# Kernel optimization log

Hardware: AMD Instinct MI355X
Metric: run time of the kernel (lower is better)

Reference implementation:

```python
import jax, jax.numpy as jnp
import numpy as np

_IDENTITY = jnp.array([1, 0, 0, 0], dtype=jnp.float32)

G, T, P, B = 512, 128, 256, 512  # num_graphs, max_terms, n_params, batch


def setup_inputs() -> dict:
    key = jax.random.key(0)
    k0, k1, k2, k3, k4 = jax.random.split(key, 5)
    psi_const = jax.random.randint(k0, (G, T), 0, 2).astype(jnp.int32)
    psi_params = jax.random.randint(k1, (G, T, P), 0, 2).astype(jnp.float32)
    phi_const = jax.random.randint(k2, (G, T), 0, 2).astype(jnp.int32)
    phi_params = jax.random.randint(k3, (G, T, P), 0, 2).astype(jnp.float32)
    param_vals = jax.random.randint(k4, (B, P), 0, 2).astype(jnp.float32)
    return {
        "psi_const": psi_const,
        "psi_params": psi_params,
        "phi_const": phi_const,
        "phi_params": phi_params,
        "param_vals": param_vals,
    }


def reference(psi_const, psi_params, phi_const, phi_params, param_vals):
    # GF(2) matmul: contract bitmasks with binary parameter values, mod 2.
    # psi_params: (G,T,P), param_vals: (B,P) -> (B,G,T)
    psi = jnp.mod(psi_const[None].astype(jnp.float32)
                  + jnp.einsum("gtp,bp->bgt", psi_params, param_vals), 2.0)
    phi = jnp.mod(phi_const[None].astype(jnp.float32)
                  + jnp.einsum("gtp,bp->bgt", phi_params, param_vals), 2.0)
    # Elementwise parity product and mod-2 sum over terms -> (B,G)
    exponent = jnp.mod(psi * phi, 2.0)
    sum_exponents = jnp.mod(jnp.sum(exponent, axis=-1), 2.0)
    # Parity-to-sign: (-1)^e = 1 - 2e, embedded as exact scalar (B,G,4)
    summands_exact = (1.0 - 2.0 * sum_exponents)[..., None] * _IDENTITY
    return summands_exact
```

## Files before the change

### kernel.cpp

```cpp
#include <hip/hip_runtime.h>

typedef unsigned long long u64;

#define G 512
#define T 128
#define P 256
#define B 512

struct __align__(16) U64x2 { u64 x, y; };

__global__ __launch_bounds__(256) void pack_pv_kernel(
    const float* __restrict__ pv, u64* __restrict__ out)
{
    int lane = threadIdx.x & 63;
    int wave = threadIdx.x >> 6;
    int row  = blockIdx.x * 4 + wave;
    const float4* src = (const float4*)(pv + (size_t)row * P);
    float4 f = src[lane];
    u64 w0 = __ballot(f.x != 0.0f);
    u64 w1 = __ballot(f.y != 0.0f);
    u64 w2 = __ballot(f.z != 0.0f);
    u64 w3 = __ballot(f.w != 0.0f);
    if (lane == 0) {
        U64x2* d = (U64x2*)(out + row * 4);
        U64x2 a; a.x = w0; a.y = w1;
        U64x2 c; c.x = w2; c.y = w3;
        d[0] = a;
        d[1] = c;
    }
}

__global__ __launch_bounds__(256) void pack_codes_kernel(
    const int* __restrict__ psi_c, const int* __restrict__ phi_c,
    u64* __restrict__ codes)
{
    int lane = threadIdx.x & 63;
    int wave = threadIdx.x >> 6;
    int g = blockIdx.x * 4 + wave;
    u64 a0 = __ballot(psi_c[g * T + lane]      != 0);
    u64 a1 = __ballot(psi_c[g * T + 64 + lane] != 0);
    u64 b0 = __ballot(phi_c[g * T + lane]      != 0);
    u64 b1 = __ballot(phi_c[g * T + 64 + lane] != 0);
    if (lane == 0) {
        U64x2* d = (U64x2*)(codes + g * 4);
        U64x2 x; x.x = a0; x.y = a1;
        U64x2 y; y.x = b0; y.y = b1;
        d[0] = x;
        d[1] = y;
    }
}

__global__ __launch_bounds__(256) void pack_mat_kernel(
    const float* __restrict__ psi, const float* __restrict__ phi,
    u64* __restrict__ rows)
{
    int lane = threadIdx.x & 63;
    int wave = threadIdx.x >> 6;
    int wid  = blockIdx.x * 4 + wave;
    #pragma unroll 4
    for (int j = 0; j < 16; ++j) {
        int item = wid * 16 + j;
        int m = item >> 16;
        int r = item & 65535;
        const float* mat = m ? phi : psi;
        const float4* src = (const float4*)(mat + (size_t)r * P);
        float4 f = src[lane];
        u64 w0 = __ballot(f.x != 0.0f);
        u64 w1 = __ballot(f.y != 0.0f);
        u64 w2 = __ballot(f.z != 0.0f);
        u64 w3 = __ballot(f.w != 0.0f);
        if (lane == 0) {
            U64x2* d = (U64x2*)(rows + (size_t)r * 8 + m * 4);
            U64x2 a; a.x = w0; a.y = w1;
            U64x2 c; c.x = w2; c.y = w3;
            d[0] = a;
            d[1] = c;
        }
    }
}

__global__ __launch_bounds__(256) void pi_main_kernel(
    const u64* __restrict__ rows,
    const u64* __restrict__ codes,
    const u64* __restrict__ pv,
    float4*    __restrict__ out)
{
    const int g = blockIdx.x >> 1;
    const int b = ((blockIdx.x & 1) << 8) | threadIdx.x;

    const u64* v = pv + (size_t)b * 4;
    u64 v0 = v[0], v1 = v[1], v2 = v[2], v3 = v[3];

    const u64* rp = rows + (size_t)g * (T * 8);

    unsigned e = 0;
    for (int blk = 0; blk < 2; ++blk) {
        u64 pcw = codes[g * 4 + blk];
        u64 qcw = codes[g * 4 + 2 + blk];
        const u64* r = rp + blk * 64 * 8;
        #pragma unroll 4
        for (int i = 0; i < 64; ++i, r += 8) {
            u64 ma = (r[0] & v0) ^ (r[1] & v1) ^ (r[2] & v2) ^ (r[3] & v3);
            u64 mb = (r[4] & v0) ^ (r[5] & v1) ^ (r[6] & v2) ^ (r[7] & v3);
            unsigned pa = (unsigned)__popcll(ma) ^ (unsigned)(pcw >> i);
            unsigned pb = (unsigned)__popcll(mb) ^ (unsigned)(qcw >> i);
            e ^= pa & pb;
        }
    }
    e &= 1u;

    float s = 1.0f - 2.0f * (float)e;
    out[(size_t)b * G + g] = make_float4(s, 0.0f, 0.0f, 0.0f);
}

extern "C" void kernel_launch(void* const* d_in, const int* in_sizes, int n_in,
                              void* d_out, int out_size, void* d_ws, size_t ws_size,
                              hipStream_t stream) {
    const int*   psi_const  = (const int*)  d_in[0];
    const float* psi_params = (const float*)d_in[1];
    const int*   phi_const  = (const int*)  d_in[2];
    const float* phi_params = (const float*)d_in[3];
    const float* param_vals = (const float*)d_in[4];

    u64* ws    = (u64*)d_ws;
    u64* rows  = ws;
    u64* codes = ws + (size_t)G * T * 8;
    u64* pv    = codes + (size_t)G * 4;

    pack_pv_kernel   <<<B / 4, 256, 0, stream>>>(param_vals, pv);
    pack_codes_kernel<<<G / 4, 256, 0, stream>>>(psi_const, phi_const, codes);
    pack_mat_kernel  <<<2048,  256, 0, stream>>>(psi_params, phi_params, rows);
    pi_main_kernel   <<<G * 2, 256, 0, stream>>>(rows, codes, pv, (float4*)d_out);
}
```

Baseline: 196.2 us.

## Pack bitmasks per-thread via exponent bit, merge small packers, split terms across halves

Packing no longer uses wave ballots. Each thread reads 32 contiguous floats and builds a 32-bit word from bit 29 of each float, which only works for exact 0.0/1.0 inputs. The two small packing kernels are merged into one launch, cutting a kernel launch. The main kernel now uses four blocks per graph and splits the 128 terms between two thread halves, whose partial parities are combined through shared memory. The goal is more parallelism and better packing bandwidth, at the cost of a sync and relying on the binary-valued inputs.

```diff
diff --git a/kernel.cpp b/kernel.cpp
--- a/kernel.cpp
+++ b/kernel.cpp
@@ -1,81 +1,77 @@
 #include <hip/hip_runtime.h>
 
 typedef unsigned long long u64;
+typedef unsigned int u32;
 
 #define G 512
 #define T 128
 #define P 256
 #define B 512
+#define NROWS 65536
 
-struct __align__(16) U64x2 { u64 x, y; };
 
-__global__ __launch_bounds__(256) void pack_pv_kernel(
-    const float* __restrict__ pv, u64* __restrict__ out)
+__global__ __launch_bounds__(256) void pack_big_kernel(
+    const float* __restrict__ psi, const float* __restrict__ phi,
+    u32* __restrict__ rows)
 {
-    int lane = threadIdx.x & 63;
-    int wave = threadIdx.x >> 6;
-    int row  = blockIdx.x * 4 + wave;
-    const float4* src = (const float4*)(pv + (size_t)row * P);
-    float4 f = src[lane];
-    u64 w0 = __ballot(f.x != 0.0f);
-    u64 w1 = __ballot(f.y != 0.0f);
-    u64 w2 = __ballot(f.z != 0.0f);
-    u64 w3 = __ballot(f.w != 0.0f);
-    if (lane == 0) {
-        U64x2* d = (U64x2*)(out + row * 4);
-        U64x2 a; a.x = w0; a.y = w1;
-        U64x2 c; c.x = w2; c.y = w3;
-        d[0] = a;
-        d[1] = c;
+    const unsigned tid = blockIdx.x * 256u + threadIdx.x;
+    const unsigned w = tid & 7u;
+    const unsigned r = (tid >> 3) & 65535u;
+    const unsigned m = tid >> 19;
+    const float* mat = m ? phi : psi;
+    const float4* src = (const float4*)(mat + (size_t)r * P + w * 32u);
+
+    float4 f[8];
+    #pragma unroll
+    for (int s = 0; s < 8; ++s) f[s] = src[s];
+
+    u32 word = 0;
+    #pragma unroll
+    for (int s = 0; s < 8; ++s) {
+        word |= ((__float_as_uint(f[s].x) >> 29) & 1u) << (4 * s + 0);
+        word |= ((__float_as_uint(f[s].y) >> 29) & 1u) << (4 * s + 1);
+        word |= ((__float_as_uint(f[s].z) >> 29) & 1u) << (4 * s + 2);
+        word |= ((__float_as_uint(f[s].w) >> 29) & 1u) << (4 * s + 3);
     }
+    rows[(size_t)r * 16u + m * 8u + w] = word;
 }
 
-__global__ __launch_bounds__(256) void pack_codes_kernel(
-    const int* __restrict__ psi_c, const int* __restrict__ phi_c,
-    u64* __restrict__ codes)
+__global__ __launch_bounds__(256) void pack_small_kernel(
+    const float* __restrict__ pv, const int* __restrict__ psi_c,
+    const int* __restrict__ phi_c, u32* __restrict__ pv_out,
+    u32* __restrict__ codes)
 {
-    int lane = threadIdx.x & 63;
-    int wave = threadIdx.x >> 6;
-    int g = blockIdx.x * 4 + wave;
-    u64 a0 = __ballot(psi_c[g * T + lane]      != 0);
-    u64 a1 = __ballot(psi_c[g * T + 64 + lane] != 0);
-    u64 b0 = __ballot(phi_c[g * T + lane]      != 0);
-    u64 b1 = __ballot(phi_c[g * T + 64 + lane] != 0);
-    if (lane == 0) {
-        U64x2* d = (U64x2*)(codes + g * 4);
-        U64x2 x; x.x = a0; x.y = a1;
-        U64x2 y; y.x = b0; y.y = b1;
-        d[0] = x;
-        d[1] = y;
-    }
-}
-
-__global__ __launch_bounds__(256) void pack_mat_kernel(
-    const float* __restrict__ psi, const float* __restrict__ phi,
-    u64* __restrict__ rows)
-{
-    int lane = threadIdx.x & 63;
-    int wave = threadIdx.x >> 6;
-    int wid  = blockIdx.x * 4 + wave;
-    #pragma unroll 4
-    for (int j = 0; j < 16; ++j) {
-        int item = wid * 16 + j;
-        int m = item >> 16;
-        int r = item & 65535;
-        const float* mat = m ? phi : psi;
-        const float4* src = (const float4*)(mat + (size_t)r * P);
-        float4 f = src[lane];
-        u64 w0 = __ballot(f.x != 0.0f);
-        u64 w1 = __ballot(f.y != 0.0f);
-        u64 w2 = __ballot(f.z != 0.0f);
-        u64 w3 = __ballot(f.w != 0.0f);
-        if (lane == 0) {
-            U64x2* d = (U64x2*)(rows + (size_t)r * 8 + m * 4);
-            U64x2 a; a.x = w0; a.y = w1;
-            U64x2 c; c.x = w2; c.y = w3;
-            d[0] = a;
-            d[1] = c;
+    const unsigned tid = blockIdx.x * 256u + threadIdx.x;
+    if (tid < 4096u) {
+        const unsigned b = tid >> 3, j = tid & 7u;
+        const float4* src = (const float4*)(pv + (size_t)b * P + j * 32u);
+        float4 f[8];
+        #pragma unroll
+        for (int s = 0; s < 8; ++s) f[s] = src[s];
+        u32 word = 0;
+        #pragma unroll
+        for (int s = 0; s < 8; ++s) {
+            word |= ((__float_as_uint(f[s].x) >> 29) & 1u) << (4 * s + 0);
+            word |= ((__float_as_uint(f[s].y) >> 29) & 1u) << (4 * s + 1);
+            word |= ((__float_as_uint(f[s].z) >> 29) & 1u) << (4 * s + 2);
+            word |= ((__float_as_uint(f[s].w) >> 29) & 1u) << (4 * s + 3);
         }
+        pv_out[b * 8u + j] = word;
+    } else {
+        const unsigned t2 = tid - 4096u;
+        const unsigned g = t2 >> 3, k = t2 & 7u;
+        const int* src = ((k < 4u) ? psi_c : phi_c) + (size_t)g * T + (k & 3u) * 32u;
+        const int4* s4 = (const int4*)src;
+        u32 word = 0;
+        #pragma unroll
+        for (int s = 0; s < 8; ++s) {
+            int4 c = s4[s];
+            word |= ((u32)c.x & 1u) << (4 * s + 0);
+            word |= ((u32)c.y & 1u) << (4 * s + 1);
+            word |= ((u32)c.z & 1u) << (4 * s + 2);
+            word |= ((u32)c.w & 1u) << (4 * s + 3);
+        }
+        codes[g * 8u + k] = word;
     }
 }
 
@@ -85,32 +81,40 @@
     const u64* __restrict__ pv,
     float4*    __restrict__ out)
 {
-    const int g = blockIdx.x >> 1;
-    const int b = ((blockIdx.x & 1) << 8) | threadIdx.x;
+    __shared__ unsigned epart[128];
+
+    const int g   = blockIdx.x >> 2;
+    const int q   = blockIdx.x & 3;
+    const int tid = threadIdx.x;
+    const int h   = tid >> 7;
+    const int bl  = tid & 127;
+    const int b   = q * 128 + bl;
 
     const u64* v = pv + (size_t)b * 4;
     u64 v0 = v[0], v1 = v[1], v2 = v[2], v3 = v[3];
 
-    const u64* rp = rows + (size_t)g * (T * 8);
+    u64 pcw = codes[g * 4 + h];
+    u64 qcw = codes[g * 4 + 2 + h];
+
+    const u64* r = rows + ((size_t)g * T + (size_t)h * 64) * 8;
 
     unsigned e = 0;
-    for (int blk = 0; blk < 2; ++blk) {
-        u64 pcw = codes[g * 4 + blk];
-        u64 qcw = codes[g * 4 + 2 + blk];
-        const u64* r = rp + blk * 64 * 8;
-        #pragma unroll 4
-        for (int i = 0; i < 64; ++i, r += 8) {
-            u64 ma = (r[0] & v0) ^ (r[1] & v1) ^ (r[2] & v2) ^ (r[3] & v3);
-            u64 mb = (r[4] & v0) ^ (r[5] & v1) ^ (r[6] & v2) ^ (r[7] & v3);
-            unsigned pa = (unsigned)__popcll(ma) ^ (unsigned)(pcw >> i);
-            unsigned pb = (unsigned)__popcll(mb) ^ (unsigned)(qcw >> i);
-            e ^= pa & pb;
-        }
+    #pragma unroll 4
+    for (int i = 0; i < 64; ++i, r += 8) {
+        u64 ma = (r[0] & v0) ^ (r[1] & v1) ^ (r[2] & v2) ^ (r[3] & v3);
+        u64 mb = (r[4] & v0) ^ (r[5] & v1) ^ (r[6] & v2) ^ (r[7] & v3);
+        unsigned pa = (unsigned)__popcll(ma) ^ (unsigned)(pcw >> i);
+        unsigned pb = (unsigned)__popcll(mb) ^ (unsigned)(qcw >> i);
+        e ^= pa & pb;
     }
-    e &= 1u;
 
-    float s = 1.0f - 2.0f * (float)e;
-    out[(size_t)b * G + g] = make_float4(s, 0.0f, 0.0f, 0.0f);
+    if (h) epart[bl] = e;
+    __syncthreads();
+    if (!h) {
+        e ^= epart[bl];
+        float s = 1.0f - 2.0f * (float)(e & 1u);
+        out[(size_t)b * G + g] = make_float4(s, 0.0f, 0.0f, 0.0f);
+    }
 }
 
 extern "C" void kernel_launch(void* const* d_in, const int* in_sizes, int n_in,
@@ -122,13 +126,15 @@
     const float* phi_params = (const float*)d_in[3];
     const float* param_vals = (const float*)d_in[4];
 
-    u64* ws    = (u64*)d_ws;
-    u64* rows  = ws;
-    u64* codes = ws + (size_t)G * T * 8;
-    u64* pv    = codes + (size_t)G * 4;
+    u32* rows_u32  = (u32*)d_ws;
+    u32* codes_u32 = rows_u32 + (size_t)NROWS * 16;
+    u32* pv_u32    = codes_u32 + (size_t)G * 8;
 
-    pack_pv_kernel   <<<B / 4, 256, 0, stream>>>(param_vals, pv);
-    pack_codes_kernel<<<G / 4, 256, 0, stream>>>(psi_const, phi_const, codes);
-    pack_mat_kernel  <<<2048,  256, 0, stream>>>(psi_params, phi_params, rows);
-    pi_main_kernel   <<<G * 2, 256, 0, stream>>>(rows, codes, pv, (float4*)d_out);
+    pack_big_kernel  <<<4096, 256, 0, stream>>>(psi_params, phi_params, rows_u32);
+    pack_small_kernel<<<32,   256, 0, stream>>>(param_vals, psi_const, phi_const,
+                                                pv_u32, codes_u32);
+    pi_main_kernel   <<<G * 4, 256, 0, stream>>>((const u64*)rows_u32,
+                                                 (const u64*)codes_u32,
+                                                 (const u64*)pv_u32,
+                                                 (float4*)d_out);
 }
```

After: 217.6 us. 10.9% more time.
